# Kernel optimization log

Hardware: AMD Instinct MI355X
Metric: run time of the kernel (lower is better)

Reference implementation:

```python
import jax, jax.numpy as jnp
import numpy as np

B, S, F, H, C, L = 256, 128, 128, 512, 64, 16


def setup_inputs() -> dict:
    key = jax.random.key(0)
    ks = jax.random.split(key, 16)
    stdv = 1.0 / np.sqrt(H)
    u = lambda k, shape, s=stdv: jax.random.uniform(k, shape, jnp.float32, -s, s)
    W_ih = u(ks[0], (F, 4 * H))
    b_ih = u(ks[1], (4 * H,)).at[H:2 * H].set(1.0)  # forget-gate bias init = 1
    W_hh = u(ks[2], (H, 4 * H))
    b_hh = u(ks[3], (4 * H,)).at[H:2 * H].set(1.0)
    cg_w1 = u(ks[4], (C, H))
    cg_b1 = u(ks[5], (H,))
    cg_w2 = u(ks[6], (H, 3 * H))
    cg_b2 = jnp.ones((3 * H,), jnp.float32)  # context_gate[-2].bias.fill_(1.0)
    mu_w = u(ks[7], (H, L))
    mu_b = u(ks[8], (L,))
    lv_w = u(ks[9], (H, L))
    lv_b = u(ks[10], (L,))
    dec_w1 = u(ks[11], (L, H))
    dec_b1 = u(ks[12], (H,))
    dec_w2 = u(ks[13], (H, F))
    dec_b2 = u(ks[14], (F,))
    kx, kc, ke = jax.random.split(ks[15], 3)
    return dict(
        x=jax.random.normal(kx, (B, S, F), jnp.float32),
        context=jax.random.normal(kc, (B, C), jnp.float32),
        eps=jax.random.normal(ke, (B, L), jnp.float32),
        W_ih=W_ih, b_ih=b_ih, W_hh=W_hh, b_hh=b_hh,
        cg_w1=cg_w1, cg_b1=cg_b1, cg_w2=cg_w2, cg_b2=cg_b2,
        mu_w=mu_w, mu_b=mu_b, lv_w=lv_w, lv_b=lv_b,
        dec_w1=dec_w1, dec_b1=dec_b1, dec_w2=dec_w2, dec_b2=dec_b2,
    )


def reference(x, context, eps, W_ih, b_ih, W_hh, b_hh, cg_w1, cg_b1, cg_w2, cg_b2,
              mu_w, mu_b, lv_w, lv_b, dec_w1, dec_b1, dec_w2, dec_b2):
    Bsz, Slen, _ = x.shape
    Hd = W_hh.shape[0]
    # context is static across time -> context-gate computed once (same math as
    # recomputing identically at each step)
    ctx = jax.nn.sigmoid(jax.nn.relu(context @ cg_w1 + cg_b1) @ cg_w2 + cg_b2)  # [B, 3H]
    ci, cf, co = jnp.split(ctx, 3, axis=1)
    # precompute input projections for all timesteps: [S, B, 4H]
    xg = jnp.einsum('bsf,fk->sbk', x, W_ih) + b_ih

    def step(carry, xg_t):
        h, c = carry
        gates = xg_t + h @ W_hh + b_hh
        i, f, g, o = jnp.split(gates, 4, axis=1)
        i = jax.nn.sigmoid(i) * ci
        f = jax.nn.sigmoid(f) * cf
        g = jnp.tanh(g)
        o = jax.nn.sigmoid(o) * co
        c_next = f * c + i * g
        h_next = o * jnp.tanh(c_next)
        return (h_next, c_next), None

    h0 = jnp.zeros((Bsz, Hd), x.dtype)
    (h, _), _ = jax.lax.scan(step, (h0, h0), xg)

    mu = h @ mu_w + mu_b
    log_var = h @ lv_w + lv_b
    z = mu + eps * jnp.exp(0.5 * log_var)  # reparameterize
    recon_x = jax.nn.relu(z @ dec_w1 + dec_b1) @ dec_w2 + dec_b2
    return recon_x, mu, log_var
```

## Files before the change

kernel.cpp:

```cpp
#include <hip/hip_runtime.h>
#include <cstdint>
#include <cstddef>

#define B_ 256
#define S_ 128
#define F_ 128
#define H_ 512
#define C_ 64
#define L_ 16

typedef __attribute__((ext_vector_type(8))) short short8;
typedef __attribute__((ext_vector_type(4))) float f4;
typedef __attribute__((ext_vector_type(4))) unsigned int u4;

__device__ __forceinline__ unsigned short f2bf(float f) {
  union { float f; unsigned u; } v; v.f = f;
  unsigned r = v.u + 0x7fffu + ((v.u >> 16) & 1u);
  return (unsigned short)(r >> 16);
}
__device__ __forceinline__ float sigmoid_(float x) { return 1.0f / (1.0f + __expf(-x)); }
__device__ __forceinline__ float tanh_(float x) {
  x = fminf(15.f, fmaxf(-15.f, x));
  float e = __expf(2.f * x);
  return (e - 1.f) / (e + 1.f);
}

__global__ void prepack_w(const float* __restrict__ W_hh, const float* __restrict__ W_ih,
                          const float* __restrict__ b_ih, const float* __restrict__ b_hh,
                          unsigned short* __restrict__ Wpk, unsigned short* __restrict__ Wipk,
                          float* __restrict__ bc) {
  int t = blockIdx.x * blockDim.x + threadIdx.x;
  if (t < 131072) {
    int lane = t & 63, row = t >> 6;
    int kit = row & 15, gh = row >> 4;
    int g = gh & 3, ht = gh >> 2;
    int k0 = kit * 32 + ((lane >> 4) << 3);
    int col = g * 512 + ht * 16 + (lane & 15);
#pragma unroll
    for (int j = 0; j < 8; j++)
      Wpk[t * 8 + j] = f2bf(W_hh[(k0 + j) * 2048 + col]);
  } else if (t < 131072 + 32768) {
    int t2 = t - 131072;
    int lane = t2 & 63, row = t2 >> 6;
    int kit = row & 3, gh = row >> 2;
    int g = gh & 3, ht = gh >> 2;
    int k0 = kit * 32 + ((lane >> 4) << 3);
    int col = g * 512 + ht * 16 + (lane & 15);
#pragma unroll
    for (int j = 0; j < 8; j++)
      Wipk[t2 * 8 + j] = f2bf(W_ih[(k0 + j) * 2048 + col]);
  } else if (t < 131072 + 32768 + 2048) {
    int i = t - 131072 - 32768;
    bc[i] = b_ih[i] + b_hh[i];
  }
}

__global__ void prepack_x(const float* __restrict__ x, unsigned short* __restrict__ xfr) {
  int o8 = blockIdx.x * blockDim.x + threadIdx.x;
  int m = o8 & 15, kb = (o8 >> 4) & 15, Rg = (o8 >> 8) & 15, s = o8 >> 12;
  int b = Rg * 16 + m;
  const float* src = x + (b * S_ + s) * F_ + kb * 8;
  unsigned short* dst = xfr + o8 * 8;
#pragma unroll
  for (int j = 0; j < 8; j++) dst[j] = f2bf(src[j]);
}

__global__ void ctx1_kernel(const float* __restrict__ context, const float* __restrict__ w1,
                            const float* __restrict__ b1, float* __restrict__ hid1) {
  __shared__ float cc[C_];
  int b = blockIdx.x, t = threadIdx.x;
  if (t < C_) cc[t] = context[b * C_ + t];
  __syncthreads();
  for (int j = t; j < H_; j += 256) {
    float acc = b1[j];
#pragma unroll 8
    for (int k = 0; k < C_; k++) acc = fmaf(cc[k], w1[k * H_ + j], acc);
    hid1[b * H_ + j] = fmaxf(acc, 0.f);
  }
}

__global__ void ctx2_kernel(const float* __restrict__ hid1, const float* __restrict__ w2,
                            const float* __restrict__ b2, float* __restrict__ ctxg) {
  __shared__ float hr[4 * H_];
  int r0 = blockIdx.x * 4, t = threadIdx.x;
  for (int i = t; i < 4 * H_; i += 256) hr[i] = hid1[r0 * H_ + i];
  __syncthreads();
  float acc[4][6];
#pragma unroll
  for (int r = 0; r < 4; r++)
#pragma unroll
    for (int i = 0; i < 6; i++) acc[r][i] = 0.f;
  for (int k = 0; k < H_; k++) {
    float w[6];
#pragma unroll
    for (int i = 0; i < 6; i++) w[i] = w2[k * 1536 + t + i * 256];
#pragma unroll
    for (int r = 0; r < 4; r++) {
      float hv = hr[r * H_ + k];
#pragma unroll
      for (int i = 0; i < 6; i++) acc[r][i] = fmaf(hv, w[i], acc[r][i]);
    }
  }
#pragma unroll
  for (int r = 0; r < 4; r++)
#pragma unroll
    for (int i = 0; i < 6; i++) {
      int col = t + i * 256;
      ctxg[(r0 + r) * 1536 + col] = sigmoid_(acc[r][i] + b2[col]);
    }
}

__global__ void __launch_bounds__(256) lstm_kernel(
    const unsigned short* __restrict__ xfr, const unsigned short* __restrict__ Wpk,
    const unsigned short* __restrict__ Wipk, const float* __restrict__ bc,
    const float* __restrict__ ctxg, float* __restrict__ hfinal,
    unsigned short* __restrict__ hb0, unsigned short* __restrict__ hb1,
    unsigned int* __restrict__ ctr) {
  __shared__ __align__(16) unsigned short lds_h[16384];
  __shared__ __align__(16) unsigned short lds_x[4096];
  __shared__ float lds_g[128 * 17];

  int tid = threadIdx.x, lane = tid & 63, wid = tid >> 6;
  int bt = blockIdx.x >> 5, ht = blockIdx.x & 31;

  short8 wf[16], wfi[4];
  {
    const short8* wp = (const short8*)Wpk + (ht * 4 + wid) * 16 * 64 + lane;
#pragma unroll
    for (int kit = 0; kit < 16; kit++) wf[kit] = wp[kit * 64];
    const short8* wip = (const short8*)Wipk + (ht * 4 + wid) * 4 * 64 + lane;
#pragma unroll
    for (int kit = 0; kit < 4; kit++) wfi[kit] = wip[kit * 64];
  }

  int bl = tid >> 3, jl0 = (tid & 7) * 2;
  int bglob = bt * 32 + bl;
  int j0 = ht * 16 + jl0;
  float cst[2] = {0.f, 0.f};
  float ci_[2], cf_[2], co_[2], bi_[2], bf_[2], bg_[2], bo_[2];
#pragma unroll
  for (int p = 0; p < 2; p++) {
    int j = j0 + p;
    ci_[p] = ctxg[bglob * 1536 + j];
    cf_[p] = ctxg[bglob * 1536 + 512 + j];
    co_[p] = ctxg[bglob * 1536 + 1024 + j];
    bi_[p] = bc[j]; bf_[p] = bc[512 + j]; bg_[p] = bc[1024 + j]; bo_[p] = bc[1536 + j];
  }
  int hoff2 = (((bt * 2 + (bl >> 4)) * 64 + ht * 2 + (jl0 >> 3)) * 128
               + (bl & 15) * 8 + (jl0 & 7)) >> 1;

#pragma unroll
  for (int i = 0; i < 2; i++) {
    int c = wid * 2 + i, R = c >> 2, kit = c & 3;
    u4 d = *(const u4*)(xfr + (size_t)((bt * 2 + R) * 16 + kit * 4) * 128 + lane * 8);
    *(u4*)(lds_x + (R * 4 + kit) * 512 + lane * 8) = d;
  }
  __syncthreads();

  for (int t = 0; t < S_; t++) {
    const unsigned short* hread = (t & 1) ? hb1 : hb0;
    unsigned short* hwrite = (t & 1) ? hb0 : hb1;

    if (t > 0) {
      const unsigned int* cb = ctr + (unsigned)((t - 1) * 8 + bt) * 256;
      for (;;) {
        unsigned a = __hip_atomic_load(cb,       __ATOMIC_RELAXED, __HIP_MEMORY_SCOPE_AGENT);
        unsigned b = __hip_atomic_load(cb + 64,  __ATOMIC_RELAXED, __HIP_MEMORY_SCOPE_AGENT);
        unsigned c = __hip_atomic_load(cb + 128, __ATOMIC_RELAXED, __HIP_MEMORY_SCOPE_AGENT);
        unsigned d = __hip_atomic_load(cb + 192, __ATOMIC_RELAXED, __HIP_MEMORY_SCOPE_AGENT);
        if (a + b + c + d >= 128u) break;
      }
    }

    u4 tmp[8];
#pragma unroll
    for (int i = 0; i < 8; i++) {
      int c = wid * 8 + i, R = c >> 4, kit = c & 15;
      const unsigned int* src = (const unsigned int*)hread
          + (bt * 2 + R) * 4096 + kit * 256 + lane * 4;
      asm volatile("global_load_dwordx4 %0, %1, off sc0 sc1"
                   : "=v"(tmp[i]) : "v"(src) : "memory");
    }

    f4 acc0 = {0.f, 0.f, 0.f, 0.f}, acc1 = {0.f, 0.f, 0.f, 0.f};
#pragma unroll
    for (int kit = 0; kit < 4; kit++) {
      short8 a0 = *(const short8*)(lds_x + kit * 512 + lane * 8);
      short8 a1 = *(const short8*)(lds_x + 2048 + kit * 512 + lane * 8);
      acc0 = __builtin_amdgcn_mfma_f32_16x16x32_bf16(a0, wfi[kit], acc0, 0, 0, 0);
      acc1 = __builtin_amdgcn_mfma_f32_16x16x32_bf16(a1, wfi[kit], acc1, 0, 0, 0);
    }

    asm volatile("s_waitcnt vmcnt(0)"
                 : "+v"(tmp[0]), "+v"(tmp[1]), "+v"(tmp[2]), "+v"(tmp[3]),
                   "+v"(tmp[4]), "+v"(tmp[5]), "+v"(tmp[6]), "+v"(tmp[7])
                 :: "memory");
#pragma unroll
    for (int i = 0; i < 8; i++) {
      int c = wid * 8 + i, R = c >> 4, kit = c & 15;
      *(u4*)(lds_h + R * 8192 + kit * 512 + lane * 8) = tmp[i];
    }
    __syncthreads();

#pragma unroll
    for (int kit = 0; kit < 16; kit++) {
      short8 a0 = *(const short8*)(lds_h + kit * 512 + lane * 8);
      short8 a1 = *(const short8*)(lds_h + 8192 + kit * 512 + lane * 8);
      acc0 = __builtin_amdgcn_mfma_f32_16x16x32_bf16(a0, wf[kit], acc0, 0, 0, 0);
      acc1 = __builtin_amdgcn_mfma_f32_16x16x32_bf16(a1, wf[kit], acc1, 0, 0, 0);
    }

    {
      int q = lane >> 4, n = lane & 15;
#pragma unroll
      for (int r = 0; r < 4; r++) {
        lds_g[(wid * 32 + q * 4 + r) * 17 + n] = acc0[r];
        lds_g[(wid * 32 + 16 + q * 4 + r) * 17 + n] = acc1[r];
      }
    }
    __syncthreads();

    {
      float hv[2];
#pragma unroll
      for (int p = 0; p < 2; p++) {
        int jl = jl0 + p;
        float gi = lds_g[(0 * 32 + bl) * 17 + jl] + bi_[p];
        float gf = lds_g[(1 * 32 + bl) * 17 + jl] + bf_[p];
        float gg = lds_g[(2 * 32 + bl) * 17 + jl] + bg_[p];
        float go = lds_g[(3 * 32 + bl) * 17 + jl] + bo_[p];
        float iv = ci_[p] * sigmoid_(gi);
        float fv = cf_[p] * sigmoid_(gf);
        float ov = co_[p] * sigmoid_(go);
        float gv = tanh_(gg);
        float c = fv * cst[p] + iv * gv;
        cst[p] = c;
        hv[p] = ov * tanh_(c);
      }
      unsigned int packed = (unsigned)f2bf(hv[0]) | ((unsigned)f2bf(hv[1]) << 16);
      unsigned int* dst = (unsigned int*)hwrite + hoff2;
      asm volatile("global_store_dword %0, %1, off sc0 sc1"
                   :: "v"(dst), "v"(packed) : "memory");
      if (t == S_ - 1) {
        hfinal[bglob * H_ + j0] = hv[0];
        hfinal[bglob * H_ + j0 + 1] = hv[1];
      }
    }

    if (t < S_ - 1) {
      asm volatile("s_waitcnt vmcnt(0)" ::: "memory");
      if (lane == 0)
        __hip_atomic_fetch_add(ctr + (unsigned)(t * 8 + bt) * 256 + wid * 64, 1u,
                               __ATOMIC_RELAXED, __HIP_MEMORY_SCOPE_AGENT);
#pragma unroll
      for (int i = 0; i < 2; i++) {
        int c = wid * 2 + i, R = c >> 2, kit = c & 3;
        u4 d = *(const u4*)(xfr + (size_t)((((t + 1) * 16) + bt * 2 + R) * 16 + kit * 4) * 128 + lane * 8);
        *(u4*)(lds_x + (R * 4 + kit) * 512 + lane * 8) = d;
      }
    }
    __syncthreads();
  }
}

__global__ void post_kernel(const float* __restrict__ hfinal, const float* __restrict__ eps,
                            const float* __restrict__ mu_w, const float* __restrict__ mu_b,
                            const float* __restrict__ lv_w, const float* __restrict__ lv_b,
                            const float* __restrict__ dw1, const float* __restrict__ db1,
                            const float* __restrict__ dw2, const float* __restrict__ db2,
                            float* __restrict__ out) {
  __shared__ float sh[H_], sh1[H_], smu[L_], slv[L_], sz[L_];
  int b = blockIdx.x, t = threadIdx.x;
  for (int i = t; i < H_; i += 256) sh[i] = hfinal[b * H_ + i];
  __syncthreads();
  {
    int o = t >> 3, sub = t & 7, l = o & 15;
    const float* w = (o < 16) ? mu_w : lv_w;
    float acc = 0.f;
    int k0 = sub * 64;
#pragma unroll 8
    for (int k = k0; k < k0 + 64; k++) acc = fmaf(sh[k], w[k * L_ + l], acc);
#pragma unroll
    for (int d = 4; d >= 1; d >>= 1) acc += __shfl_down(acc, d, 8);
    if (sub == 0) {
      if (o < 16) { float v = acc + mu_b[l]; smu[l] = v; out[32768 + b * 16 + l] = v; }
      else        { float v = acc + lv_b[l]; slv[l] = v; out[36864 + b * 16 + l] = v; }
    }
  }
  __syncthreads();
  if (t < L_) sz[t] = smu[t] + eps[b * L_ + t] * __expf(0.5f * slv[t]);
  __syncthreads();
  for (int j = t; j < H_; j += 256) {
    float acc = db1[j];
#pragma unroll
    for (int l = 0; l < L_; l++) acc = fmaf(sz[l], dw1[l * H_ + j], acc);
    sh1[j] = fmaxf(acc, 0.f);
  }
  __syncthreads();
  if (t < F_) {
    float acc = db2[t];
    for (int k = 0; k < H_; k++) acc = fmaf(sh1[k], dw2[k * F_ + t], acc);
    out[b * F_ + t] = acc;
  }
}

extern "C" void kernel_launch(void* const* d_in, const int* in_sizes, int n_in,
                              void* d_out, int out_size, void* d_ws, size_t ws_size,
                              hipStream_t stream) {
  const float* x      = (const float*)d_in[0];
  const float* ctxin  = (const float*)d_in[1];
  const float* eps    = (const float*)d_in[2];
  const float* W_ih   = (const float*)d_in[3];
  const float* b_ih   = (const float*)d_in[4];
  const float* W_hh   = (const float*)d_in[5];
  const float* b_hh   = (const float*)d_in[6];
  const float* cg_w1  = (const float*)d_in[7];
  const float* cg_b1  = (const float*)d_in[8];
  const float* cg_w2  = (const float*)d_in[9];
  const float* cg_b2  = (const float*)d_in[10];
  const float* mu_w   = (const float*)d_in[11];
  const float* mu_b   = (const float*)d_in[12];
  const float* lv_w   = (const float*)d_in[13];
  const float* lv_b   = (const float*)d_in[14];
  const float* dec_w1 = (const float*)d_in[15];
  const float* dec_b1 = (const float*)d_in[16];
  const float* dec_w2 = (const float*)d_in[17];
  const float* dec_b2 = (const float*)d_in[18];
  float* out = (float*)d_out;

  char* ws = (char*)d_ws;
  size_t off = 0;
  auto alloc = [&](size_t bytes) { char* p = ws + off; off = (off + bytes + 255) & ~(size_t)255; return p; };

  unsigned short* hb0 = (unsigned short*)alloc(B_ * H_ * 2);
  unsigned short* hb1 = (unsigned short*)alloc(B_ * H_ * 2);
  unsigned int*   ctr = (unsigned int*)alloc(128 * 8 * 256 * 4);
  size_t zero_bytes = off;
  unsigned short* xfr  = (unsigned short*)alloc((size_t)B_ * S_ * F_ * 2);
  unsigned short* Wpk  = (unsigned short*)alloc((size_t)H_ * 2048 * 2);
  unsigned short* Wipk = (unsigned short*)alloc((size_t)F_ * 2048 * 2);
  float* bc    = (float*)alloc(2048 * 4);
  float* ctxg  = (float*)alloc((size_t)B_ * 1536 * 4);
  float* hid1  = (float*)alloc((size_t)B_ * H_ * 4);
  float* hfin  = (float*)alloc((size_t)B_ * H_ * 4);
  (void)ws_size; (void)in_sizes; (void)n_in; (void)out_size;

  hipMemsetAsync(d_ws, 0, zero_bytes, stream);

  prepack_w<<<648, 256, 0, stream>>>(W_hh, W_ih, b_ih, b_hh, Wpk, Wipk, bc);
  prepack_x<<<2048, 256, 0, stream>>>(x, xfr);
  ctx1_kernel<<<256, 256, 0, stream>>>(ctxin, cg_w1, cg_b1, hid1);
  ctx2_kernel<<<64, 256, 0, stream>>>(hid1, cg_w2, cg_b2, ctxg);
  lstm_kernel<<<256, 256, 0, stream>>>(xfr, Wpk, Wipk, bc, ctxg, hfin, hb0, hb1, ctr);
  post_kernel<<<256, 256, 0, stream>>>(hfin, eps, mu_w, mu_b, lv_w, lv_b,
                                       dec_w1, dec_b1, dec_w2, dec_b2, out);
}
```

Measured before the change: 569.5 us.

## Repartition LSTM blocks so each wave owns all four gates of its columns

The LSTM grid goes from 256 blocks (32 batch rows by 16 hidden columns) to 128 blocks (16 batch rows by 64 hidden columns). Each wave now holds the W_hh and W_ih fragments for all four gates of its 16 columns in registers. Gate activations can then be combined directly from MFMA accumulators, which removes the LDS gate-exchange buffer and one barrier per step. The x tile is loaded straight into registers instead of staged through LDS, and the per-step synchronisation waits on fewer arrivals per batch tile. The cost is much higher register pressure (80 short8 weight fragments per lane) and half as many blocks in the grid.

After: 785.1 us. 1.38x slower.

```diff
diff --git a/kernel.cpp b/kernel.cpp
--- a/kernel.cpp
+++ b/kernel.cpp
@@ -31,21 +31,21 @@
                           float* __restrict__ bc) {
   int t = blockIdx.x * blockDim.x + threadIdx.x;
   if (t < 131072) {
-    int lane = t & 63, row = t >> 6;
-    int kit = row & 15, gh = row >> 4;
-    int g = gh & 3, ht = gh >> 2;
+    int lane = t & 63, r = t >> 6;
+    int kit = r & 15, z = r >> 4;
+    int gate = z & 3, w = (z >> 2) & 3, g = z >> 4;
+    int col = gate * 512 + g * 64 + w * 16 + (lane & 15);
     int k0 = kit * 32 + ((lane >> 4) << 3);
-    int col = g * 512 + ht * 16 + (lane & 15);
 #pragma unroll
     for (int j = 0; j < 8; j++)
       Wpk[t * 8 + j] = f2bf(W_hh[(k0 + j) * 2048 + col]);
   } else if (t < 131072 + 32768) {
     int t2 = t - 131072;
-    int lane = t2 & 63, row = t2 >> 6;
-    int kit = row & 3, gh = row >> 2;
-    int g = gh & 3, ht = gh >> 2;
+    int lane = t2 & 63, r = t2 >> 6;
+    int kit = r & 3, z = r >> 2;
+    int gate = z & 3, w = (z >> 2) & 3, g = z >> 4;
+    int col = gate * 512 + g * 64 + w * 16 + (lane & 15);
     int k0 = kit * 32 + ((lane >> 4) << 3);
-    int col = g * 512 + ht * 16 + (lane & 15);
 #pragma unroll
     for (int j = 0; j < 8; j++)
       Wipk[t2 * 8 + j] = f2bf(W_ih[(k0 + j) * 2048 + col]);
@@ -110,154 +110,134 @@
     }
 }
 
-__global__ void __launch_bounds__(256) lstm_kernel(
+__global__ void __launch_bounds__(256, 1) lstm_kernel(
     const unsigned short* __restrict__ xfr, const unsigned short* __restrict__ Wpk,
     const unsigned short* __restrict__ Wipk, const float* __restrict__ bc,
     const float* __restrict__ ctxg, float* __restrict__ hfinal,
     unsigned short* __restrict__ hb0, unsigned short* __restrict__ hb1,
     unsigned int* __restrict__ ctr) {
-  __shared__ __align__(16) unsigned short lds_h[16384];
-  __shared__ __align__(16) unsigned short lds_x[4096];
-  __shared__ float lds_g[128 * 17];
+  __shared__ __align__(16) unsigned short lds_h[8192];
 
   int tid = threadIdx.x, lane = tid & 63, wid = tid >> 6;
-  int bt = blockIdx.x >> 5, ht = blockIdx.x & 31;
-
-  short8 wf[16], wfi[4];
-  {
-    const short8* wp = (const short8*)Wpk + (ht * 4 + wid) * 16 * 64 + lane;
-#pragma unroll
-    for (int kit = 0; kit < 16; kit++) wf[kit] = wp[kit * 64];
-    const short8* wip = (const short8*)Wipk + (ht * 4 + wid) * 4 * 64 + lane;
-#pragma unroll
-    for (int kit = 0; kit < 4; kit++) wfi[kit] = wip[kit * 64];
-  }
-
-  int bl = tid >> 3, jl0 = (tid & 7) * 2;
-  int bglob = bt * 32 + bl;
-  int j0 = ht * 16 + jl0;
-  float cst[2] = {0.f, 0.f};
-  float ci_[2], cf_[2], co_[2], bi_[2], bf_[2], bg_[2], bo_[2];
-#pragma unroll
-  for (int p = 0; p < 2; p++) {
-    int j = j0 + p;
-    ci_[p] = ctxg[bglob * 1536 + j];
-    cf_[p] = ctxg[bglob * 1536 + 512 + j];
-    co_[p] = ctxg[bglob * 1536 + 1024 + j];
-    bi_[p] = bc[j]; bf_[p] = bc[512 + j]; bg_[p] = bc[1024 + j]; bo_[p] = bc[1536 + j];
-  }
-  int hoff2 = (((bt * 2 + (bl >> 4)) * 64 + ht * 2 + (jl0 >> 3)) * 128
-               + (bl & 15) * 8 + (jl0 & 7)) >> 1;
-
-#pragma unroll
-  for (int i = 0; i < 2; i++) {
-    int c = wid * 2 + i, R = c >> 2, kit = c & 3;
-    u4 d = *(const u4*)(xfr + (size_t)((bt * 2 + R) * 16 + kit * 4) * 128 + lane * 8);
-    *(u4*)(lds_x + (R * 4 + kit) * 512 + lane * 8) = d;
-  }
-  __syncthreads();
+  int bt = blockIdx.x >> 3, g = blockIdx.x & 7;
+
+  short8 wf[4][16], wfi[4][4];
+#pragma unroll
+  for (int gate = 0; gate < 4; gate++) {
+    const short8* wp = (const short8*)Wpk + (size_t)((g * 16 + wid * 4 + gate) * 16) * 64 + lane;
+#pragma unroll
+    for (int kit = 0; kit < 16; kit++) wf[gate][kit] = wp[kit * 64];
+    const short8* wip = (const short8*)Wipk + (size_t)((g * 16 + wid * 4 + gate) * 4) * 64 + lane;
+#pragma unroll
+    for (int kit = 0; kit < 4; kit++) wfi[gate][kit] = wip[kit * 64];
+  }
+
+  int q = lane >> 4, n = lane & 15;
+  int colglob = g * 64 + wid * 16 + n;
+  float ci_[4], cf_[4], co_[4], cst[4] = {0.f, 0.f, 0.f, 0.f};
+#pragma unroll
+  for (int r = 0; r < 4; r++) {
+    int brow = bt * 16 + q * 4 + r;
+    ci_[r] = ctxg[brow * 1536 + colglob];
+    cf_[r] = ctxg[brow * 1536 + 512 + colglob];
+    co_[r] = ctxg[brow * 1536 + 1024 + colglob];
+  }
+  float bi = bc[colglob], bff = bc[512 + colglob], bgg = bc[1024 + colglob], bo = bc[1536 + colglob];
+
+  int hsub = (bt * 16 + (colglob >> 5)) * 512 + ((colglob >> 3) & 3) * 128 + (colglob & 7);
 
   for (int t = 0; t < S_; t++) {
     const unsigned short* hread = (t & 1) ? hb1 : hb0;
     unsigned short* hwrite = (t & 1) ? hb0 : hb1;
 
     if (t > 0) {
-      const unsigned int* cb = ctr + (unsigned)((t - 1) * 8 + bt) * 256;
+      const unsigned int* cb = ctr + (unsigned)((t - 1) * 16 + bt) * 256;
       for (;;) {
         unsigned a = __hip_atomic_load(cb,       __ATOMIC_RELAXED, __HIP_MEMORY_SCOPE_AGENT);
         unsigned b = __hip_atomic_load(cb + 64,  __ATOMIC_RELAXED, __HIP_MEMORY_SCOPE_AGENT);
         unsigned c = __hip_atomic_load(cb + 128, __ATOMIC_RELAXED, __HIP_MEMORY_SCOPE_AGENT);
         unsigned d = __hip_atomic_load(cb + 192, __ATOMIC_RELAXED, __HIP_MEMORY_SCOPE_AGENT);
-        if (a + b + c + d >= 128u) break;
+        if (a + b + c + d >= 32u) break;
       }
     }
 
-    u4 tmp[8];
-#pragma unroll
-    for (int i = 0; i < 8; i++) {
-      int c = wid * 8 + i, R = c >> 4, kit = c & 15;
-      const unsigned int* src = (const unsigned int*)hread
-          + (bt * 2 + R) * 4096 + kit * 256 + lane * 4;
-      asm volatile("global_load_dwordx4 %0, %1, off sc0 sc1"
-                   : "=v"(tmp[i]) : "v"(src) : "memory");
-    }
-
-    f4 acc0 = {0.f, 0.f, 0.f, 0.f}, acc1 = {0.f, 0.f, 0.f, 0.f};
+    u4 xt[4];
+#pragma unroll
+    for (int kit = 0; kit < 4; kit++)
+      xt[kit] = *(const u4*)(xfr + ((size_t)(t * 16 + bt) * 4 + kit) * 512 + lane * 8);
+
+    u4 t0, t1, t2, t3;
+    {
+      const unsigned int* hbase = (const unsigned int*)hread + (bt * 16 + wid * 4) * 256 + lane * 4;
+      const unsigned int* a0 = hbase;
+      const unsigned int* a1 = hbase + 256;
+      const unsigned int* a2 = hbase + 512;
+      const unsigned int* a3 = hbase + 768;
+      asm volatile(
+          "global_load_dwordx4 %0, %4, off sc0 sc1\n\t"
+          "global_load_dwordx4 %1, %5, off sc0 sc1\n\t"
+          "global_load_dwordx4 %2, %6, off sc0 sc1\n\t"
+          "global_load_dwordx4 %3, %7, off sc0 sc1\n\t"
+          "s_waitcnt vmcnt(0)"
+          : "=&v"(t0), "=&v"(t1), "=&v"(t2), "=&v"(t3)
+          : "v"(a0), "v"(a1), "v"(a2), "v"(a3)
+          : "memory");
+    }
+    *(u4*)(lds_h + (wid * 4 + 0) * 512 + lane * 8) = t0;
+    *(u4*)(lds_h + (wid * 4 + 1) * 512 + lane * 8) = t1;
+    *(u4*)(lds_h + (wid * 4 + 2) * 512 + lane * 8) = t2;
+    *(u4*)(lds_h + (wid * 4 + 3) * 512 + lane * 8) = t3;
+    __syncthreads();
+
+    f4 acc[4];
+#pragma unroll
+    for (int gate = 0; gate < 4; gate++) acc[gate] = (f4){0.f, 0.f, 0.f, 0.f};
 #pragma unroll
     for (int kit = 0; kit < 4; kit++) {
-      short8 a0 = *(const short8*)(lds_x + kit * 512 + lane * 8);
-      short8 a1 = *(const short8*)(lds_x + 2048 + kit * 512 + lane * 8);
-      acc0 = __builtin_amdgcn_mfma_f32_16x16x32_bf16(a0, wfi[kit], acc0, 0, 0, 0);
-      acc1 = __builtin_amdgcn_mfma_f32_16x16x32_bf16(a1, wfi[kit], acc1, 0, 0, 0);
-    }
-
-    asm volatile("s_waitcnt vmcnt(0)"
-                 : "+v"(tmp[0]), "+v"(tmp[1]), "+v"(tmp[2]), "+v"(tmp[3]),
-                   "+v"(tmp[4]), "+v"(tmp[5]), "+v"(tmp[6]), "+v"(tmp[7])
-                 :: "memory");
-#pragma unroll
-    for (int i = 0; i < 8; i++) {
-      int c = wid * 8 + i, R = c >> 4, kit = c & 15;
-      *(u4*)(lds_h + R * 8192 + kit * 512 + lane * 8) = tmp[i];
-    }
-    __syncthreads();
+      short8 a = __builtin_bit_cast(short8, xt[kit]);
+#pragma unroll
+      for (int gate = 0; gate < 4; gate++)
+        acc[gate] = __builtin_amdgcn_mfma_f32_16x16x32_bf16(a, wfi[gate][kit], acc[gate], 0, 0, 0);
+    }
 
 #pragma unroll
     for (int kit = 0; kit < 16; kit++) {
-      short8 a0 = *(const short8*)(lds_h + kit * 512 + lane * 8);
-      short8 a1 = *(const short8*)(lds_h + 8192 + kit * 512 + lane * 8);
-      acc0 = __builtin_amdgcn_mfma_f32_16x16x32_bf16(a0, wf[kit], acc0, 0, 0, 0);
-      acc1 = __builtin_amdgcn_mfma_f32_16x16x32_bf16(a1, wf[kit], acc1, 0, 0, 0);
-    }
-
-    {
-      int q = lane >> 4, n = lane & 15;
-#pragma unroll
-      for (int r = 0; r < 4; r++) {
-        lds_g[(wid * 32 + q * 4 + r) * 17 + n] = acc0[r];
-        lds_g[(wid * 32 + 16 + q * 4 + r) * 17 + n] = acc1[r];
-      }
-    }
-    __syncthreads();
-
-    {
-      float hv[2];
-#pragma unroll
-      for (int p = 0; p < 2; p++) {
-        int jl = jl0 + p;
-        float gi = lds_g[(0 * 32 + bl) * 17 + jl] + bi_[p];
-        float gf = lds_g[(1 * 32 + bl) * 17 + jl] + bf_[p];
-        float gg = lds_g[(2 * 32 + bl) * 17 + jl] + bg_[p];
-        float go = lds_g[(3 * 32 + bl) * 17 + jl] + bo_[p];
-        float iv = ci_[p] * sigmoid_(gi);
-        float fv = cf_[p] * sigmoid_(gf);
-        float ov = co_[p] * sigmoid_(go);
-        float gv = tanh_(gg);
-        float c = fv * cst[p] + iv * gv;
-        cst[p] = c;
-        hv[p] = ov * tanh_(c);
-      }
-      unsigned int packed = (unsigned)f2bf(hv[0]) | ((unsigned)f2bf(hv[1]) << 16);
-      unsigned int* dst = (unsigned int*)hwrite + hoff2;
-      asm volatile("global_store_dword %0, %1, off sc0 sc1"
-                   :: "v"(dst), "v"(packed) : "memory");
-      if (t == S_ - 1) {
-        hfinal[bglob * H_ + j0] = hv[0];
-        hfinal[bglob * H_ + j0 + 1] = hv[1];
-      }
+      short8 a = *(const short8*)(lds_h + kit * 512 + lane * 8);
+#pragma unroll
+      for (int gate = 0; gate < 4; gate++)
+        acc[gate] = __builtin_amdgcn_mfma_f32_16x16x32_bf16(a, wf[gate][kit], acc[gate], 0, 0, 0);
+    }
+
+    float hv[4];
+#pragma unroll
+    for (int r = 0; r < 4; r++) {
+      float gi = acc[0][r] + bi, gf = acc[1][r] + bff, gc = acc[2][r] + bgg, go = acc[3][r] + bo;
+      float iv = ci_[r] * sigmoid_(gi);
+      float fv = cf_[r] * sigmoid_(gf);
+      float ov = co_[r] * sigmoid_(go);
+      float gv = tanh_(gc);
+      float c = fv * cst[r] + iv * gv;
+      cst[r] = c;
+      hv[r] = ov * tanh_(c);
+    }
+
+#pragma unroll
+    for (int r = 0; r < 4; r++) {
+      unsigned short* d = hwrite + hsub + (q * 4 + r) * 8;
+      unsigned hb = (unsigned)f2bf(hv[r]);
+      asm volatile("global_store_short %0, %1, off sc0 sc1" :: "v"(d), "v"(hb) : "memory");
+    }
+    if (t == S_ - 1) {
+#pragma unroll
+      for (int r = 0; r < 4; r++)
+        hfinal[(bt * 16 + q * 4 + r) * H_ + colglob] = hv[r];
     }
 
     if (t < S_ - 1) {
       asm volatile("s_waitcnt vmcnt(0)" ::: "memory");
       if (lane == 0)
-        __hip_atomic_fetch_add(ctr + (unsigned)(t * 8 + bt) * 256 + wid * 64, 1u,
+        __hip_atomic_fetch_add(ctr + (unsigned)(t * 16 + bt) * 256 + wid * 64, 1u,
                                __ATOMIC_RELAXED, __HIP_MEMORY_SCOPE_AGENT);
-#pragma unroll
-      for (int i = 0; i < 2; i++) {
-        int c = wid * 2 + i, R = c >> 2, kit = c & 3;
-        u4 d = *(const u4*)(xfr + (size_t)((((t + 1) * 16) + bt * 2 + R) * 16 + kit * 4) * 128 + lane * 8);
-        *(u4*)(lds_x + (R * 4 + kit) * 512 + lane * 8) = d;
-      }
     }
     __syncthreads();
   }
@@ -334,7 +314,7 @@
 
   unsigned short* hb0 = (unsigned short*)alloc(B_ * H_ * 2);
   unsigned short* hb1 = (unsigned short*)alloc(B_ * H_ * 2);
-  unsigned int*   ctr = (unsigned int*)alloc(128 * 8 * 256 * 4);
+  unsigned int*   ctr = (unsigned int*)alloc(128 * 16 * 256 * 4);
   size_t zero_bytes = off;
   unsigned short* xfr  = (unsigned short*)alloc((size_t)B_ * S_ * F_ * 2);
   unsigned short* Wpk  = (unsigned short*)alloc((size_t)H_ * 2048 * 2);
@@ -351,7 +331,7 @@
   prepack_x<<<2048, 256, 0, stream>>>(x, xfr);
   ctx1_kernel<<<256, 256, 0, stream>>>(ctxin, cg_w1, cg_b1, hid1);
   ctx2_kernel<<<64, 256, 0, stream>>>(hid1, cg_w2, cg_b2, ctxg);
-  lstm_kernel<<<256, 256, 0, stream>>>(xfr, Wpk, Wipk, bc, ctxg, hfin, hb0, hb1, ctr);
+  lstm_kernel<<<128, 256, 0, stream>>>(xfr, Wpk, Wipk, bc, ctxg, hfin, hb0, hb1, ctr);
   post_kernel<<<256, 256, 0, stream>>>(hfin, eps, mu_w, mu_b, lv_w, lv_b,
                                        dec_w1, dec_b1, dec_w2, dec_b2, out);
 }
```
